# Optimization experiments

Measured on AMD Instinct MI355X. Metric: run time of the kernel, lower is better.

Reference implementation:

```python
import jax, jax.numpy as jnp
import numpy as np
from jax import lax

T = 300       # windowsize
F = 39        # input features
H1, H2 = 35, 30
FC1, FC2, OUT = 50, 40, 2
B = 4096


def _glorot(key, shape):
    fan_in, fan_out = shape[0], shape[1]
    lim = np.sqrt(6.0 / (fan_in + fan_out)).astype(np.float32)
    return jax.random.uniform(key, shape, jnp.float32, -lim, lim)


def setup_inputs() -> dict:
    key = jax.random.key(0)
    ks = jax.random.split(key, 16)
    inp = {"x": jax.random.normal(ks[0], (B, T, F), jnp.float32)}
    # LSTM weights: W [in+h, 4h] with TF gate order (i, j, f, o), bias zeros
    inp["w_fw1"] = _glorot(ks[1], (F + H1, 4 * H1)); inp["b_fw1"] = jnp.zeros((4 * H1,), jnp.float32)
    inp["w_fw2"] = _glorot(ks[2], (H1 + H2, 4 * H2)); inp["b_fw2"] = jnp.zeros((4 * H2,), jnp.float32)
    inp["w_bw1"] = _glorot(ks[3], (F + H1, 4 * H1)); inp["b_bw1"] = jnp.zeros((4 * H1,), jnp.float32)
    inp["w_bw2"] = _glorot(ks[4], (H1 + H2, 4 * H2)); inp["b_bw2"] = jnp.zeros((4 * H2,), jnp.float32)
    inp["w_fc1"] = _glorot(ks[5], (2 * H2, FC1)); inp["b_fc1"] = jnp.zeros((FC1,), jnp.float32)
    inp["w_fc2"] = _glorot(ks[6], (FC1, FC2));    inp["b_fc2"] = jnp.zeros((FC2,), jnp.float32)
    inp["w_fc3"] = _glorot(ks[7], (FC2, OUT));    inp["b_fc3"] = jnp.zeros((OUT,), jnp.float32)
    return inp


def _lstm(x_tbi, W, b, h):
    # TF LSTMCell math: z = [x,h]@W + b; gates i, j, f, o; forget_bias=1.0
    bsz = x_tbi.shape[1]
    init = (jnp.zeros((bsz, h), x_tbi.dtype), jnp.zeros((bsz, h), x_tbi.dtype))

    def step(carry, xt):
        hp, cp = carry
        z = jnp.concatenate([xt, hp], axis=-1) @ W + b
        i, j, f, o = jnp.split(z, 4, axis=-1)
        c = jax.nn.sigmoid(f + 1.0) * cp + jax.nn.sigmoid(i) * jnp.tanh(j)
        hn = jax.nn.sigmoid(o) * jnp.tanh(c)
        return (hn, c), hn

    _, ys = lax.scan(step, init, x_tbi)
    return ys  # [T, B, h]


def _forward(x, w_fw1, b_fw1, w_fw2, b_fw2, w_bw1, b_bw1, w_bw2, b_bw2,
             w_fc1, b_fc1, w_fc2, b_fc2, w_fc3, b_fc3):
    xt = jnp.transpose(x, (1, 0, 2))  # [T, B, F]
    # forward direction, 2 stacked layers
    fw = _lstm(_lstm(xt, w_fw1, b_fw1, H1), w_fw2, b_fw2, H2)
    # backward direction: reverse time, run, reverse back
    xr = xt[::-1]
    bw = _lstm(_lstm(xr, w_bw1, b_bw1, H1), w_bw2, b_bw2, H2)[::-1]
    rnn = jnp.concatenate([fw, bw], axis=-1)            # [T, B, 2*H2]
    rnn = jnp.transpose(rnn, (1, 0, 2))                 # [B, T, 2*H2]
    h = jax.nn.relu(rnn @ w_fc1 + b_fc1)
    h = jax.nn.relu(h @ w_fc2 + b_fc2)
    logits = h @ w_fc3 + b_fc3                          # [B, T, 2]
    return logits


def reference(x, w_fw1, b_fw1, w_fw2, b_fw2, w_bw1, b_bw1, w_bw2, b_bw2,
              w_fc1, b_fc1, w_fc2, b_fc2, w_fc3, b_fc3):
    return _forward(x, w_fw1, b_fw1, w_fw2, b_fw2, w_bw1, b_bw1, w_bw2, b_bw2,
                    w_fc1, b_fc1, w_fc2, b_fc2, w_fc3, b_fc3)
```

## Files before the change

### kernel.cpp

```cpp
#include <hip/hip_runtime.h>

#define TT 300
#define FF 39
#define H1C 35
#define H2C 30
#define BB 4096
#define RPB 32
#define NTH 512
#define AP 104
#define ZTP 36
#define NFC1 50
#define NFC2 40
#define RNNCH 60

typedef __attribute__((ext_vector_type(8))) short s8v;
typedef __attribute__((ext_vector_type(4))) float f4v;

__device__ __forceinline__ float sigf(float v){ return 1.0f/(1.0f+__expf(-v)); }
__device__ __forceinline__ float tanh_(float v){ return 1.0f - 2.0f/(__expf(2.0f*v)+1.0f); }

__device__ __forceinline__ unsigned short bf16rne(float f){
  unsigned u = __float_as_uint(f);
  return (unsigned short)((u + 0x7fffu + ((u>>16)&1u)) >> 16);
}
__device__ __forceinline__ void split2(float f, unsigned short& hi, unsigned short& lo){
  hi = bf16rne(f);
  float fh = __uint_as_float(((unsigned)hi)<<16);
  lo = bf16rne(f - fh);
}

__global__ __launch_bounds__(NTH, 2)
void lstm2_mfma(const float* __restrict__ x,
                const float* __restrict__ Wf1, const float* __restrict__ Bf1,
                const float* __restrict__ Wf2, const float* __restrict__ Bf2,
                const float* __restrict__ Wb1, const float* __restrict__ Bb1,
                const float* __restrict__ Wb2, const float* __restrict__ Bb2,
                float* __restrict__ rnn)
{
  __shared__ __align__(16) unsigned short A1h[RPB][AP], A1l[RPB][AP];
  __shared__ __align__(16) unsigned short A2h[RPB][AP], A2l[RPB][AP];
  __shared__ __align__(16) float zT[144][ZTP];

  const int dir = blockIdx.y;
  const int b0  = blockIdx.x * RPB;
  const float* W1 = dir ? Wb1 : Wf1; const float* B1 = dir ? Bb1 : Bf1;
  const float* W2 = dir ? Wb2 : Wf2; const float* B2 = dir ? Bb2 : Bf2;

  const int tid  = threadIdx.x;
  const int lane = tid & 63, w = tid >> 6;
  const int fr   = lane & 15, kgq = lane >> 4;

  s8v B1hf[2][3], B1lf[2][3], B2hf[3], B2lf[3];
  for (int slot = 0; slot < 2; ++slot) {
    const int nt = (slot==0) ? w : 8;
    const bool act = (slot==0) || (w==0);
    for (int kc = 0; kc < 3; ++kc) {
      s8v vh, vl;
      #pragma unroll
      for (int j = 0; j < 8; ++j) {
        float wv = 0.f;
        if (act) {
          int k = kc*32 + kgq*8 + j;
          int col = nt*16 + fr;
          int ks = (k < 39) ? k : (k >= 48 && k < 83) ? 39 + (k-48) : -1;
          if (ks >= 0 && col < 140) wv = W1[ks*140 + col];
        }
        unsigned short h_, l_; split2(wv, h_, l_);
        vh[j] = (short)h_; vl[j] = (short)l_;
      }
      B1hf[slot][kc] = vh; B1lf[slot][kc] = vl;
    }
  }
  for (int kc = 0; kc < 3; ++kc) {
    s8v vh, vl;
    #pragma unroll
    for (int j = 0; j < 8; ++j) {
      float wv = 0.f;
      int k = kc*32 + kgq*8 + j;
      int col = w*16 + fr;
      int ks = (k < 35) ? k : (k >= 48 && k < 78) ? 35 + (k-48) : -1;
      if (ks >= 0 && col < 120) wv = W2[ks*120 + col];
      unsigned short h_, l_; split2(wv, h_, l_);
      vh[j] = (short)h_; vl[j] = (short)l_;
    }
    B2hf[kc] = vh; B2lf[kc] = vl;
  }

  int k1v[3], r1v[3]; float bias1[3][4]; bool act1[3];
  #pragma unroll
  for (int s = 0; s < 3; ++s) {
    int u = tid + s*NTH; act1[s] = (u < H1C*RPB);
    int uu = act1[s] ? u : 0;
    r1v[s] = uu & 31; k1v[s] = uu >> 5;
    #pragma unroll
    for (int g = 0; g < 4; ++g) bias1[s][g] = B1[g*H1C + k1v[s]];
  }
  int k2v[2], r2v[2]; float bias2[2][4]; bool act2[2];
  #pragma unroll
  for (int s = 0; s < 2; ++s) {
    int u = tid + s*NTH; act2[s] = (u < H2C*RPB);
    int uu = act2[s] ? u : 0;
    r2v[s] = uu & 31; k2v[s] = uu >> 5;
    #pragma unroll
    for (int g = 0; g < 4; ++g) bias2[s][g] = B2[g*H2C + k2v[s]];
  }

  for (int i = tid; i < RPB*AP; i += NTH) {
    ((unsigned short*)A1h)[i] = 0; ((unsigned short*)A1l)[i] = 0;
    ((unsigned short*)A2h)[i] = 0; ((unsigned short*)A2l)[i] = 0;
  }
  __syncthreads();
  const int t0in = dir ? (TT-1) : 0;
  #pragma unroll
  for (int s = 0; s < 3; ++s) {
    int e = tid + s*NTH;
    if (e < RPB*FF) {
      int r = e/FF, c = e%FF;
      float f = x[((size_t)(b0+r)*TT + t0in)*FF + c];
      unsigned short h_, l_; split2(f, h_, l_);
      A1h[r][c] = h_; A1l[r][c] = l_;
    }
  }
  __syncthreads();

  float c1s[3] = {0.f,0.f,0.f}, c2s[2] = {0.f,0.f};

  #pragma unroll 1
  for (int t = 0; t < TT; ++t) {
    float xp[3];
    const bool pf = (t+1 < TT);
    const int tn = dir ? (TT-2-t) : (t+1);
    #pragma unroll
    for (int s = 0; s < 3; ++s) {
      xp[s] = 0.f;
      int e = tid + s*NTH;
      if (pf && e < RPB*FF)
        xp[s] = x[((size_t)(b0 + e/FF)*TT + tn)*FF + (e%FF)];
    }

    s8v a1h[2][3], a1l[2][3];
    #pragma unroll
    for (int Mt = 0; Mt < 2; ++Mt) {
      int m = Mt*16 + fr;
      #pragma unroll
      for (int kc = 0; kc < 3; ++kc) {
        int kb = kc*32 + kgq*8;
        a1h[Mt][kc] = *(const s8v*)&A1h[m][kb];
        a1l[Mt][kc] = *(const s8v*)&A1l[m][kb];
      }
    }
    for (int slot = 0; slot < 2; ++slot) {
      if (slot == 1 && w != 0) continue;
      const int nt = (slot==0) ? w : 8;
      #pragma unroll
      for (int Mt = 0; Mt < 2; ++Mt) {
        f4v acc = {0.f,0.f,0.f,0.f};
        #pragma unroll
        for (int kc = 0; kc < 3; ++kc) {
          acc = __builtin_amdgcn_mfma_f32_16x16x32_bf16(a1h[Mt][kc], B1hf[slot][kc], acc, 0,0,0);
          acc = __builtin_amdgcn_mfma_f32_16x16x32_bf16(a1h[Mt][kc], B1lf[slot][kc], acc, 0,0,0);
          acc = __builtin_amdgcn_mfma_f32_16x16x32_bf16(a1l[Mt][kc], B1hf[slot][kc], acc, 0,0,0);
        }
        *(f4v*)&zT[nt*16 + fr][Mt*16 + kgq*4] = acc;
      }
    }
    __syncthreads();

    #pragma unroll
    for (int s = 0; s < 3; ++s) {
      if (act1[s]) {
        int k = k1v[s], r = r1v[s];
        float zi = zT[k][r]       + bias1[s][0];
        float zj = zT[35+k][r]    + bias1[s][1];
        float zf = zT[70+k][r]    + bias1[s][2];
        float zo = zT[105+k][r]   + bias1[s][3];
        c1s[s] = sigf(zf + 1.f)*c1s[s] + sigf(zi)*tanh_(zj);
        float h = sigf(zo)*tanh_(c1s[s]);
        unsigned short h_, l_; split2(h, h_, l_);
        A2h[r][k] = h_;      A2l[r][k] = l_;
        A1h[r][48+k] = h_;   A1l[r][48+k] = l_;
      }
    }
    if (pf) {
      #pragma unroll
      for (int s = 0; s < 3; ++s) {
        int e = tid + s*NTH;
        if (e < RPB*FF) {
          int r = e/FF, c = e%FF;
          unsigned short h_, l_; split2(xp[s], h_, l_);
          A1h[r][c] = h_; A1l[r][c] = l_;
        }
      }
    }
    __syncthreads();

    s8v a2h[2][3], a2l[2][3];
    #pragma unroll
    for (int Mt = 0; Mt < 2; ++Mt) {
      int m = Mt*16 + fr;
      #pragma unroll
      for (int kc = 0; kc < 3; ++kc) {
        int kb = kc*32 + kgq*8;
        a2h[Mt][kc] = *(const s8v*)&A2h[m][kb];
        a2l[Mt][kc] = *(const s8v*)&A2l[m][kb];
      }
    }
    #pragma unroll
    for (int Mt = 0; Mt < 2; ++Mt) {
      f4v acc = {0.f,0.f,0.f,0.f};
      #pragma unroll
      for (int kc = 0; kc < 3; ++kc) {
        acc = __builtin_amdgcn_mfma_f32_16x16x32_bf16(a2h[Mt][kc], B2hf[kc], acc, 0,0,0);
        acc = __builtin_amdgcn_mfma_f32_16x16x32_bf16(a2h[Mt][kc], B2lf[kc], acc, 0,0,0);
        acc = __builtin_amdgcn_mfma_f32_16x16x32_bf16(a2l[Mt][kc], B2hf[kc], acc, 0,0,0);
      }
      *(f4v*)&zT[w*16 + fr][Mt*16 + kgq*4] = acc;
    }
    __syncthreads();

    const int tout = dir ? (TT-1-t) : t;
    #pragma unroll
    for (int s = 0; s < 2; ++s) {
      if (act2[s]) {
        int k = k2v[s], r = r2v[s];
        float zi = zT[k][r]      + bias2[s][0];
        float zj = zT[30+k][r]   + bias2[s][1];
        float zf = zT[60+k][r]   + bias2[s][2];
        float zo = zT[90+k][r]   + bias2[s][3];
        c2s[s] = sigf(zf + 1.f)*c2s[s] + sigf(zi)*tanh_(zj);
        float h = sigf(zo)*tanh_(c2s[s]);
        unsigned short h_, l_; split2(h, h_, l_);
        A2h[r][48+k] = h_; A2l[r][48+k] = l_;
        rnn[(((size_t)(b0+r)*TT) + tout)*RNNCH + dir*H2C + k] = h;
      }
    }
    __syncthreads();
  }
}

__global__ __launch_bounds__(256)
void fc_kernel(const float* __restrict__ rnn,
               const float* __restrict__ W1, const float* __restrict__ B1,
               const float* __restrict__ W2, const float* __restrict__ B2,
               const float* __restrict__ W3, const float* __restrict__ B3,
               float* __restrict__ out)
{
    __shared__ float w1s[RNNCH][52];
    __shared__ float w2s[NFC1*NFC2];
    __shared__ float w3s[NFC2*2];
    __shared__ float b1s[NFC1], b2s[NFC2], b3s[2];
    const int tid = threadIdx.x;
    for (int i = tid; i < RNNCH*NFC1; i += 256) w1s[i/NFC1][i%NFC1] = W1[i];
    for (int i = tid; i < NFC1*NFC2; i += 256) w2s[i] = W2[i];
    for (int i = tid; i < NFC2*2;   i += 256) w3s[i] = W3[i];
    if (tid < NFC1) b1s[tid] = B1[tid];
    if (tid < NFC2) b2s[tid] = B2[tid];
    if (tid < 2)    b3s[tid] = B3[tid];
    __syncthreads();

    const size_t row = (size_t)blockIdx.x*256 + tid;
    const float* __restrict__ in = rnn + row*RNNCH;

    float h[NFC1];
    #pragma unroll
    for (int j = 0; j < NFC1; ++j) h[j] = b1s[j];
    #pragma unroll 4
    for (int c = 0; c < RNNCH; ++c) {
        float v = in[c];
        #pragma unroll
        for (int j = 0; j < NFC1; ++j) h[j] += v * w1s[c][j];
    }
    #pragma unroll
    for (int j = 0; j < NFC1; ++j) h[j] = fmaxf(h[j], 0.0f);

    float h2[NFC2];
    #pragma unroll
    for (int j = 0; j < NFC2; ++j) h2[j] = b2s[j];
    #pragma unroll
    for (int c = 0; c < NFC1; ++c) {
        float v = h[c];
        #pragma unroll
        for (int j = 0; j < NFC2; ++j) h2[j] += v * w2s[c*NFC2 + j];
    }
    #pragma unroll
    for (int j = 0; j < NFC2; ++j) h2[j] = fmaxf(h2[j], 0.0f);

    float o0 = b3s[0], o1 = b3s[1];
    #pragma unroll
    for (int c = 0; c < NFC2; ++c) {
        o0 += h2[c] * w3s[c*2];
        o1 += h2[c] * w3s[c*2+1];
    }
    ((float2*)out)[row] = make_float2(o0, o1);
}

extern "C" void kernel_launch(void* const* d_in, const int* in_sizes, int n_in,
                              void* d_out, int out_size, void* d_ws, size_t ws_size,
                              hipStream_t stream) {
    (void)in_sizes; (void)n_in; (void)out_size; (void)ws_size;
    const float* x     = (const float*)d_in[0];
    const float* w_fw1 = (const float*)d_in[1];
    const float* b_fw1 = (const float*)d_in[2];
    const float* w_fw2 = (const float*)d_in[3];
    const float* b_fw2 = (const float*)d_in[4];
    const float* w_bw1 = (const float*)d_in[5];
    const float* b_bw1 = (const float*)d_in[6];
    const float* w_bw2 = (const float*)d_in[7];
    const float* b_bw2 = (const float*)d_in[8];
    const float* w_fc1 = (const float*)d_in[9];
    const float* b_fc1 = (const float*)d_in[10];
    const float* w_fc2 = (const float*)d_in[11];
    const float* b_fc2 = (const float*)d_in[12];
    const float* w_fc3 = (const float*)d_in[13];
    const float* b_fc3 = (const float*)d_in[14];
    float* out = (float*)d_out;

    float* rnn = (float*)d_ws;

    dim3 gl(BB/RPB, 2);
    lstm2_mfma<<<gl, NTH, 0, stream>>>(x, w_fw1, b_fw1, w_fw2, b_fw2,
                                       w_bw1, b_bw1, w_bw2, b_bw2, rnn);

    const int total = BB * TT;
    fc_kernel<<<total/256, 256, 0, stream>>>(rnn, w_fc1, b_fc1, w_fc2, b_fc2,
                                             w_fc3, b_fc3, out);
}
```

Measured before the change: 1.456 ms.

## Interleave gate columns so each lane owns its gates, drop zT and barriers

Permutes LSTM weight columns so the four gates of one hidden unit fall into one MFMA accumulator quad, then transposes them in registers with DPP so each lane runs the cell update directly from its accumulator. The zT shared staging buffer and two of the four per-step barriers go away, and the A buffers are double-buffered by step parity. Work is also split as 2 M-tiles by 4 N-groups per wave. The FC kernel now reads weights straight from global memory through uniform loads instead of LDS, and stages h1 in LDS to lower register pressure, which may cost it some performance.

```diff
diff --git a/kernel.cpp b/kernel.cpp
--- a/kernel.cpp
+++ b/kernel.cpp
@@ -8,7 +8,6 @@
 #define RPB 32
 #define NTH 512
 #define AP 104
-#define ZTP 36
 #define NFC1 50
 #define NFC2 40
 #define RNNCH 60
@@ -27,6 +26,25 @@
   hi = bf16rne(f);
   float fh = __uint_as_float(((unsigned)hi)<<16);
   lo = bf16rne(f - fh);
+}
+
+template<int CTRL>
+__device__ __forceinline__ float dppq(float v){
+  return __int_as_float(__builtin_amdgcn_update_dpp(0, __float_as_int(v), CTRL, 0xF, 0xF, true));
+}
+__device__ __forceinline__ void tr4(float&a0,float&a1,float&a2,float&a3,int q){
+  float t0=dppq<0xB1>(a1), t1=dppq<0xB1>(a0), t2=dppq<0xB1>(a3), t3=dppq<0xB1>(a2);
+  bool g0 = (q & 1);
+  a0 = g0 ? t0 : a0;
+  a1 = g0 ? a1 : t1;
+  a2 = g0 ? t2 : a2;
+  a3 = g0 ? a3 : t3;
+  float s0=dppq<0x4E>(a2), s1=dppq<0x4E>(a3), s2=dppq<0x4E>(a0), s3=dppq<0x4E>(a1);
+  bool g1 = (q & 2);
+  a0 = g1 ? s0 : a0;
+  a1 = g1 ? s1 : a1;
+  a2 = g1 ? a2 : s2;
+  a3 = g1 ? a3 : s3;
 }
 
 __global__ __launch_bounds__(NTH, 2)
@@ -37,75 +55,79 @@
                 const float* __restrict__ Wb2, const float* __restrict__ Bb2,
                 float* __restrict__ rnn)
 {
-  __shared__ __align__(16) unsigned short A1h[RPB][AP], A1l[RPB][AP];
-  __shared__ __align__(16) unsigned short A2h[RPB][AP], A2l[RPB][AP];
-  __shared__ __align__(16) float zT[144][ZTP];
+  __shared__ __align__(16) unsigned short A1h[2][RPB*AP], A1l[2][RPB*AP];
+  __shared__ __align__(16) unsigned short A2h[2][RPB*AP], A2l[2][RPB*AP];
 
   const int dir = blockIdx.y;
   const int b0  = blockIdx.x * RPB;
-  const float* W1 = dir ? Wb1 : Wf1; const float* B1 = dir ? Bb1 : Bf1;
-  const float* W2 = dir ? Wb2 : Wf2; const float* B2 = dir ? Bb2 : Bf2;
+  const float* W1  = dir ? Wb1 : Wf1; const float* B1v = dir ? Bb1 : Bf1;
+  const float* W2  = dir ? Wb2 : Wf2; const float* B2v = dir ? Bb2 : Bf2;
 
   const int tid  = threadIdx.x;
   const int lane = tid & 63, w = tid >> 6;
-  const int fr   = lane & 15, kgq = lane >> 4;
-
-  s8v B1hf[2][3], B1lf[2][3], B2hf[3], B2lf[3];
-  for (int slot = 0; slot < 2; ++slot) {
-    const int nt = (slot==0) ? w : 8;
-    const bool act = (slot==0) || (w==0);
+  const int wm = w & 1, wn = w >> 1;
+  const int fr = lane & 15, kgq = lane >> 4;
+  const int qp = lane & 3, u4 = (lane >> 2) & 3;
+
+  s8v B1h_[3][3], B1l_[3][3], B2h_[2][3], B2l_[2][3];
+  bool act1s[3];
+  #pragma unroll
+  for (int s = 0; s < 3; ++s) {
+    act1s[s] = (s < 2) || (wn == 3);
+    const int T = 2*wn + s;
+    #pragma unroll
     for (int kc = 0; kc < 3; ++kc) {
       s8v vh, vl;
       #pragma unroll
       for (int j = 0; j < 8; ++j) {
         float wv = 0.f;
-        if (act) {
+        if (act1s[s]) {
           int k = kc*32 + kgq*8 + j;
-          int col = nt*16 + fr;
-          int ks = (k < 39) ? k : (k >= 48 && k < 83) ? 39 + (k-48) : -1;
-          if (ks >= 0 && col < 140) wv = W1[ks*140 + col];
+          int col = 16*T + fr;
+          int u = col >> 2, g = col & 3;
+          int ks = (k < FF) ? k : (k >= 48 && k < 48+H1C) ? FF + (k-48) : -1;
+          if (ks >= 0 && u < H1C) wv = W1[ks*(4*H1C) + g*H1C + u];
         }
         unsigned short h_, l_; split2(wv, h_, l_);
         vh[j] = (short)h_; vl[j] = (short)l_;
       }
-      B1hf[slot][kc] = vh; B1lf[slot][kc] = vl;
-    }
-  }
-  for (int kc = 0; kc < 3; ++kc) {
-    s8v vh, vl;
-    #pragma unroll
-    for (int j = 0; j < 8; ++j) {
-      float wv = 0.f;
-      int k = kc*32 + kgq*8 + j;
-      int col = w*16 + fr;
-      int ks = (k < 35) ? k : (k >= 48 && k < 78) ? 35 + (k-48) : -1;
-      if (ks >= 0 && col < 120) wv = W2[ks*120 + col];
-      unsigned short h_, l_; split2(wv, h_, l_);
-      vh[j] = (short)h_; vl[j] = (short)l_;
-    }
-    B2hf[kc] = vh; B2lf[kc] = vl;
-  }
-
-  int k1v[3], r1v[3]; float bias1[3][4]; bool act1[3];
+      B1h_[s][kc] = vh; B1l_[s][kc] = vl;
+    }
+  }
+  #pragma unroll
+  for (int s = 0; s < 2; ++s) {
+    const int T = 2*wn + s;
+    #pragma unroll
+    for (int kc = 0; kc < 3; ++kc) {
+      s8v vh, vl;
+      #pragma unroll
+      for (int j = 0; j < 8; ++j) {
+        float wv = 0.f;
+        int k = kc*32 + kgq*8 + j;
+        int col = 16*T + fr;
+        int u = col >> 2, g = col & 3;
+        int ks = (k < H1C) ? k : (k >= 48 && k < 48+H2C) ? H1C + (k-48) : -1;
+        if (ks >= 0 && u < H2C) wv = W2[ks*(4*H2C) + g*H2C + u];
+        unsigned short h_, l_; split2(wv, h_, l_);
+        vh[j] = (short)h_; vl[j] = (short)l_;
+      }
+      B2h_[s][kc] = vh; B2l_[s][kc] = vl;
+    }
+  }
+
+  float4 bias1[3], bias2[2];
   #pragma unroll
   for (int s = 0; s < 3; ++s) {
-    int u = tid + s*NTH; act1[s] = (u < H1C*RPB);
-    int uu = act1[s] ? u : 0;
-    r1v[s] = uu & 31; k1v[s] = uu >> 5;
-    #pragma unroll
-    for (int g = 0; g < 4; ++g) bias1[s][g] = B1[g*H1C + k1v[s]];
-  }
-  int k2v[2], r2v[2]; float bias2[2][4]; bool act2[2];
+    int u = 4*(2*wn + s) + u4; int uc = u < H1C ? u : H1C-1;
+    bias1[s] = make_float4(B1v[uc], B1v[H1C+uc], B1v[2*H1C+uc], B1v[3*H1C+uc]);
+  }
   #pragma unroll
   for (int s = 0; s < 2; ++s) {
-    int u = tid + s*NTH; act2[s] = (u < H2C*RPB);
-    int uu = act2[s] ? u : 0;
-    r2v[s] = uu & 31; k2v[s] = uu >> 5;
-    #pragma unroll
-    for (int g = 0; g < 4; ++g) bias2[s][g] = B2[g*H2C + k2v[s]];
-  }
-
-  for (int i = tid; i < RPB*AP; i += NTH) {
+    int u = 4*(2*wn + s) + u4; int uc = u < H2C ? u : H2C-1;
+    bias2[s] = make_float4(B2v[uc], B2v[H2C+uc], B2v[2*H2C+uc], B2v[3*H2C+uc]);
+  }
+
+  for (int i = tid; i < 2*RPB*AP; i += NTH) {
     ((unsigned short*)A1h)[i] = 0; ((unsigned short*)A1l)[i] = 0;
     ((unsigned short*)A2h)[i] = 0; ((unsigned short*)A2l)[i] = 0;
   }
@@ -118,18 +140,22 @@
       int r = e/FF, c = e%FF;
       float f = x[((size_t)(b0+r)*TT + t0in)*FF + c];
       unsigned short h_, l_; split2(f, h_, l_);
-      A1h[r][c] = h_; A1l[r][c] = l_;
+      A1h[0][r*AP+c] = h_; A1l[0][r*AP+c] = l_;
     }
   }
   __syncthreads();
 
-  float c1s[3] = {0.f,0.f,0.f}, c2s[2] = {0.f,0.f};
+  float c1[3] = {0.f,0.f,0.f}, c2[2] = {0.f,0.f};
+  const int mrow = wm*16 + fr;
+  const int rr   = wm*16 + kgq*4 + qp;
 
   #pragma unroll 1
   for (int t = 0; t < TT; ++t) {
-    float xp[3];
+    const int p = t & 1, pn = p ^ 1;
     const bool pf = (t+1 < TT);
     const int tn = dir ? (TT-2-t) : (t+1);
+
+    float xp[3];
     #pragma unroll
     for (int s = 0; s < 3; ++s) {
       xp[s] = 0.f;
@@ -138,47 +164,34 @@
         xp[s] = x[((size_t)(b0 + e/FF)*TT + tn)*FF + (e%FF)];
     }
 
-    s8v a1h[2][3], a1l[2][3];
-    #pragma unroll
-    for (int Mt = 0; Mt < 2; ++Mt) {
-      int m = Mt*16 + fr;
-      #pragma unroll
-      for (int kc = 0; kc < 3; ++kc) {
-        int kb = kc*32 + kgq*8;
-        a1h[Mt][kc] = *(const s8v*)&A1h[m][kb];
-        a1l[Mt][kc] = *(const s8v*)&A1l[m][kb];
-      }
-    }
-    for (int slot = 0; slot < 2; ++slot) {
-      if (slot == 1 && w != 0) continue;
-      const int nt = (slot==0) ? w : 8;
-      #pragma unroll
-      for (int Mt = 0; Mt < 2; ++Mt) {
+    s8v a1hf[3], a1lf[3];
+    #pragma unroll
+    for (int kc = 0; kc < 3; ++kc) {
+      int off = mrow*AP + kc*32 + kgq*8;
+      a1hf[kc] = *(const s8v*)&A1h[p][off];
+      a1lf[kc] = *(const s8v*)&A1l[p][off];
+    }
+    #pragma unroll
+    for (int s = 0; s < 3; ++s) {
+      if (act1s[s]) {
         f4v acc = {0.f,0.f,0.f,0.f};
         #pragma unroll
         for (int kc = 0; kc < 3; ++kc) {
-          acc = __builtin_amdgcn_mfma_f32_16x16x32_bf16(a1h[Mt][kc], B1hf[slot][kc], acc, 0,0,0);
-          acc = __builtin_amdgcn_mfma_f32_16x16x32_bf16(a1h[Mt][kc], B1lf[slot][kc], acc, 0,0,0);
-          acc = __builtin_amdgcn_mfma_f32_16x16x32_bf16(a1l[Mt][kc], B1hf[slot][kc], acc, 0,0,0);
+          acc = __builtin_amdgcn_mfma_f32_16x16x32_bf16(a1hf[kc], B1h_[s][kc], acc, 0,0,0);
+          acc = __builtin_amdgcn_mfma_f32_16x16x32_bf16(a1hf[kc], B1l_[s][kc], acc, 0,0,0);
+          acc = __builtin_amdgcn_mfma_f32_16x16x32_bf16(a1lf[kc], B1h_[s][kc], acc, 0,0,0);
         }
-        *(f4v*)&zT[nt*16 + fr][Mt*16 + kgq*4] = acc;
-      }
-    }
-    __syncthreads();
-
-    #pragma unroll
-    for (int s = 0; s < 3; ++s) {
-      if (act1[s]) {
-        int k = k1v[s], r = r1v[s];
-        float zi = zT[k][r]       + bias1[s][0];
-        float zj = zT[35+k][r]    + bias1[s][1];
-        float zf = zT[70+k][r]    + bias1[s][2];
-        float zo = zT[105+k][r]   + bias1[s][3];
-        c1s[s] = sigf(zf + 1.f)*c1s[s] + sigf(zi)*tanh_(zj);
-        float h = sigf(zo)*tanh_(c1s[s]);
+        float z0 = acc[0], z1 = acc[1], z2 = acc[2], z3 = acc[3];
+        tr4(z0, z1, z2, z3, qp);
+        float zi = z0 + bias1[s].x, zj = z1 + bias1[s].y;
+        float zf = z2 + bias1[s].z, zo = z3 + bias1[s].w;
+        float cn = sigf(zf + 1.f)*c1[s] + sigf(zi)*tanh_(zj);
+        c1[s] = cn;
+        float h = sigf(zo)*tanh_(cn);
         unsigned short h_, l_; split2(h, h_, l_);
-        A2h[r][k] = h_;      A2l[r][k] = l_;
-        A1h[r][48+k] = h_;   A1l[r][48+k] = l_;
+        int u = 4*(2*wn + s) + u4;
+        A2h[p][rr*AP + u] = h_;       A2l[p][rr*AP + u] = l_;
+        A1h[pn][rr*AP + 48 + u] = h_; A1l[pn][rr*AP + 48 + u] = l_;
       }
     }
     if (pf) {
@@ -188,53 +201,42 @@
         if (e < RPB*FF) {
           int r = e/FF, c = e%FF;
           unsigned short h_, l_; split2(xp[s], h_, l_);
-          A1h[r][c] = h_; A1l[r][c] = l_;
+          A1h[pn][r*AP+c] = h_; A1l[pn][r*AP+c] = l_;
         }
       }
     }
     __syncthreads();
 
-    s8v a2h[2][3], a2l[2][3];
-    #pragma unroll
-    for (int Mt = 0; Mt < 2; ++Mt) {
-      int m = Mt*16 + fr;
-      #pragma unroll
-      for (int kc = 0; kc < 3; ++kc) {
-        int kb = kc*32 + kgq*8;
-        a2h[Mt][kc] = *(const s8v*)&A2h[m][kb];
-        a2l[Mt][kc] = *(const s8v*)&A2l[m][kb];
-      }
-    }
-    #pragma unroll
-    for (int Mt = 0; Mt < 2; ++Mt) {
+    s8v a2hf[3], a2lf[3];
+    #pragma unroll
+    for (int kc = 0; kc < 3; ++kc) {
+      int off = mrow*AP + kc*32 + kgq*8;
+      a2hf[kc] = *(const s8v*)&A2h[p][off];
+      a2lf[kc] = *(const s8v*)&A2l[p][off];
+    }
+    const int tout = dir ? (TT-1-t) : t;
+    #pragma unroll
+    for (int s = 0; s < 2; ++s) {
       f4v acc = {0.f,0.f,0.f,0.f};
       #pragma unroll
       for (int kc = 0; kc < 3; ++kc) {
-        acc = __builtin_amdgcn_mfma_f32_16x16x32_bf16(a2h[Mt][kc], B2hf[kc], acc, 0,0,0);
-        acc = __builtin_amdgcn_mfma_f32_16x16x32_bf16(a2h[Mt][kc], B2lf[kc], acc, 0,0,0);
-        acc = __builtin_amdgcn_mfma_f32_16x16x32_bf16(a2l[Mt][kc], B2hf[kc], acc, 0,0,0);
-      }
-      *(f4v*)&zT[w*16 + fr][Mt*16 + kgq*4] = acc;
-    }
-    __syncthreads();
-
-    const int tout = dir ? (TT-1-t) : t;
-    #pragma unroll
-    for (int s = 0; s < 2; ++s) {
-      if (act2[s]) {
-        int k = k2v[s], r = r2v[s];
-        float zi = zT[k][r]      + bias2[s][0];
-        float zj = zT[30+k][r]   + bias2[s][1];
-        float zf = zT[60+k][r]   + bias2[s][2];
-        float zo = zT[90+k][r]   + bias2[s][3];
-        c2s[s] = sigf(zf + 1.f)*c2s[s] + sigf(zi)*tanh_(zj);
-        float h = sigf(zo)*tanh_(c2s[s]);
-        unsigned short h_, l_; split2(h, h_, l_);
-        A2h[r][48+k] = h_; A2l[r][48+k] = l_;
-        rnn[(((size_t)(b0+r)*TT) + tout)*RNNCH + dir*H2C + k] = h;
-      }
-    }
-    __syncthreads();
+        acc = __builtin_amdgcn_mfma_f32_16x16x32_bf16(a2hf[kc], B2h_[s][kc], acc, 0,0,0);
+        acc = __builtin_amdgcn_mfma_f32_16x16x32_bf16(a2hf[kc], B2l_[s][kc], acc, 0,0,0);
+        acc = __builtin_amdgcn_mfma_f32_16x16x32_bf16(a2lf[kc], B2h_[s][kc], acc, 0,0,0);
+      }
+      float z0 = acc[0], z1 = acc[1], z2 = acc[2], z3 = acc[3];
+      tr4(z0, z1, z2, z3, qp);
+      float zi = z0 + bias2[s].x, zj = z1 + bias2[s].y;
+      float zf = z2 + bias2[s].z, zo = z3 + bias2[s].w;
+      float cn = sigf(zf + 1.f)*c2[s] + sigf(zi)*tanh_(zj);
+      c2[s] = cn;
+      float h = sigf(zo)*tanh_(cn);
+      unsigned short h_, l_; split2(h, h_, l_);
+      int u = 4*(2*wn + s) + u4;
+      A2h[pn][rr*AP + 48 + u] = h_; A2l[pn][rr*AP + 48 + u] = l_;
+      if (u < H2C)
+        rnn[(((size_t)(b0+rr)*TT) + tout)*RNNCH + dir*H2C + u] = h;
+    }
   }
 }
 
@@ -245,51 +247,41 @@
                const float* __restrict__ W3, const float* __restrict__ B3,
                float* __restrict__ out)
 {
-    __shared__ float w1s[RNNCH][52];
-    __shared__ float w2s[NFC1*NFC2];
-    __shared__ float w3s[NFC2*2];
-    __shared__ float b1s[NFC1], b2s[NFC2], b3s[2];
+    __shared__ float hbuf[256][53];
     const int tid = threadIdx.x;
-    for (int i = tid; i < RNNCH*NFC1; i += 256) w1s[i/NFC1][i%NFC1] = W1[i];
-    for (int i = tid; i < NFC1*NFC2; i += 256) w2s[i] = W2[i];
-    for (int i = tid; i < NFC2*2;   i += 256) w3s[i] = W3[i];
-    if (tid < NFC1) b1s[tid] = B1[tid];
-    if (tid < NFC2) b2s[tid] = B2[tid];
-    if (tid < 2)    b3s[tid] = B3[tid];
-    __syncthreads();
-
     const size_t row = (size_t)blockIdx.x*256 + tid;
-    const float* __restrict__ in = rnn + row*RNNCH;
+    const float4* __restrict__ inp = (const float4*)(rnn + row*RNNCH);
 
     float h[NFC1];
     #pragma unroll
-    for (int j = 0; j < NFC1; ++j) h[j] = b1s[j];
-    #pragma unroll 4
-    for (int c = 0; c < RNNCH; ++c) {
-        float v = in[c];
+    for (int j = 0; j < NFC1; ++j) h[j] = B1[j];
+    #pragma unroll 1
+    for (int s = 0; s < 15; ++s) {
+        float4 v = inp[s];
+        const float* wp = W1 + (4*s)*NFC1;
         #pragma unroll
-        for (int j = 0; j < NFC1; ++j) h[j] += v * w1s[c][j];
-    }
-    #pragma unroll
-    for (int j = 0; j < NFC1; ++j) h[j] = fmaxf(h[j], 0.0f);
+        for (int j = 0; j < NFC1; ++j)
+            h[j] += v.x*wp[j] + v.y*wp[NFC1+j] + v.z*wp[2*NFC1+j] + v.w*wp[3*NFC1+j];
+    }
+    #pragma unroll
+    for (int j = 0; j < NFC1; ++j) hbuf[tid][j] = fmaxf(h[j], 0.0f);
 
     float h2[NFC2];
     #pragma unroll
-    for (int j = 0; j < NFC2; ++j) h2[j] = b2s[j];
-    #pragma unroll
+    for (int j = 0; j < NFC2; ++j) h2[j] = B2[j];
+    #pragma unroll 1
     for (int c = 0; c < NFC1; ++c) {
-        float v = h[c];
+        float v = hbuf[tid][c];
+        const float* wp = W2 + c*NFC2;
         #pragma unroll
-        for (int j = 0; j < NFC2; ++j) h2[j] += v * w2s[c*NFC2 + j];
-    }
-    #pragma unroll
-    for (int j = 0; j < NFC2; ++j) h2[j] = fmaxf(h2[j], 0.0f);
-
-    float o0 = b3s[0], o1 = b3s[1];
+        for (int j = 0; j < NFC2; ++j) h2[j] += v*wp[j];
+    }
+
+    float o0 = B3[0], o1 = B3[1];
     #pragma unroll
     for (int c = 0; c < NFC2; ++c) {
-        o0 += h2[c] * w3s[c*2];
-        o1 += h2[c] * w3s[c*2+1];
+        float v = fmaxf(h2[c], 0.0f);
+        o0 += v*W3[2*c]; o1 += v*W3[2*c+1];
     }
     ((float2*)out)[row] = make_float2(o0, o1);
 }
```

New measurement: 1.357 ms. 1.07x faster.
